# Optimization experiments

Hardware: AMD Instinct MI355X
Metric: run time of the kernel (lower is better)

Reference implementation:

```python
import jax, jax.numpy as jnp
import numpy as np

L = 8192            # sequence length
V = 100000          # vocab size
E = 256             # embedding dim
H = 512             # lstm hidden dim (bidirectional total)
HD = H // 2         # per-direction hidden
TAGS = 32
T = TAGS + 2        # tagset + START/STOP
START = T - 2       # START_TAG = -2
STOP = T - 1        # STOP_TAG = -1
NEG = -10000.0


def setup_inputs() -> dict:
    key = jax.random.key(0)
    ks = jax.random.split(key, 11)
    s = 0.05
    return {
        "input_words": jax.random.randint(ks[0], (L,), 0, V),
        "embed": jax.random.normal(ks[1], (V, E), dtype=jnp.float32) * s,
        "Wih_f": jax.random.normal(ks[2], (4 * HD, E), dtype=jnp.float32) * s,
        "Whh_f": jax.random.normal(ks[3], (4 * HD, HD), dtype=jnp.float32) * s,
        "b_f": jax.random.normal(ks[4], (4 * HD,), dtype=jnp.float32) * s,
        "Wih_b": jax.random.normal(ks[5], (4 * HD, E), dtype=jnp.float32) * s,
        "Whh_b": jax.random.normal(ks[6], (4 * HD, HD), dtype=jnp.float32) * s,
        "b_b": jax.random.normal(ks[7], (4 * HD,), dtype=jnp.float32) * s,
        "W_out": jax.random.normal(ks[8], (T, H), dtype=jnp.float32) * s,
        "b_out": jax.random.normal(ks[9], (T,), dtype=jnp.float32) * s,
        "transitions": jax.random.normal(ks[10], (T, T), dtype=jnp.float32),
    }


def _lstm_dir(x, Wih, Whh, b, reverse):
    # single-layer LSTM, one direction; torch gate order i, f, g, o
    def step(carry, xt):
        h, c = carry
        g = xt @ Wih.T + h @ Whh.T + b
        i, f, gg, o = jnp.split(g, 4)
        i = jax.nn.sigmoid(i)
        f = jax.nn.sigmoid(f)
        gg = jnp.tanh(gg)
        o = jax.nn.sigmoid(o)
        c = f * c + i * gg
        h = o * jnp.tanh(c)
        return (h, c), h

    init = (jnp.zeros((HD,), x.dtype), jnp.zeros((HD,), x.dtype))
    _, hs = jax.lax.scan(step, init, x, reverse=reverse)
    return hs  # (L, HD)


def _crf_marginals(feats, transitions):
    lse = jax.nn.logsumexp
    # forward algorithm: alpha_t[j] = lse_i(alpha_{t-1}[i] + trans[j,i]) + feat_t[j]
    def fstep(alpha, feat):
        new = lse(alpha[None, :] + transitions, axis=1) + feat
        return new, new

    alpha0 = jnp.full((T,), NEG, feats.dtype).at[START].set(0.0)
    alphaL, log_alpha = jax.lax.scan(fstep, alpha0, feats)  # (L, T)

    # backward algorithm, replicating repo's init: beta_L[j] = lse_i(trans[i, j])
    beta_last = lse(transitions, axis=0)

    # beta_t[j] = lse_i(beta_{t+1}[i] + feat_{t+1}[i] + trans[i, j])
    def bstep(beta, feat_next):
        new = lse((beta + feat_next)[:, None] + transitions, axis=0)
        return new, new

    _, betas = jax.lax.scan(bstep, beta_last, feats[1:], reverse=True)
    log_beta = jnp.concatenate([betas, beta_last[None]], axis=0)  # (L, T)
    return log_alpha + log_beta


def reference(input_words, embed, Wih_f, Whh_f, b_f, Wih_b, Whh_b, b_b,
              W_out, b_out, transitions):
    x = embed[input_words]                           # (L, E)
    hf = _lstm_dir(x, Wih_f, Whh_f, b_f, reverse=False)
    hb = _lstm_dir(x, Wih_b, Whh_b, b_b, reverse=True)
    lstm_out = jnp.concatenate([hf, hb], axis=-1)    # (L, H)
    feats = lstm_out @ W_out.T + b_out               # (L, T)
    score = _crf_marginals(feats, transitions)       # (L, T)
    tags = jnp.argmax(score, axis=1)                 # (L,)
    return score, tags
```

## Files before the change

kernel.cpp:

```cpp
#include <hip/hip_runtime.h>
#include <cstdint>
#include <cstddef>

#define LSEQ 8192
#define NT   34
#define NP   36
#define SCH  64
#define CCH  128
#define F_L2E 1.4426950408889634f
#define F_LN2 0.6931471805599453f

#if __has_builtin(__builtin_amdgcn_sdot4)
#define DOT4(a,b,c) __builtin_amdgcn_sdot4((a),(b),(c),false)
#else
__device__ __forceinline__ int dot4_fb(int a,int b,int c){
  c += (int)(signed char)(a & 0xff)        * (int)(signed char)(b & 0xff);
  c += (int)(signed char)((a>>8) & 0xff)   * (int)(signed char)((b>>8) & 0xff);
  c += (int)(signed char)((a>>16) & 0xff)  * (int)(signed char)((b>>16) & 0xff);
  c += (a>>24) * (b>>24);
  return c;
}
#define DOT4(a,b,c) dot4_fb((a),(b),(c))
#endif

__device__ __forceinline__ float ex2(float x){
#if __has_builtin(__builtin_amdgcn_exp2f)
  return __builtin_amdgcn_exp2f(x);
#else
  return exp2f(x);
#endif
}
__device__ __forceinline__ float lg2(float x){
#if __has_builtin(__builtin_amdgcn_logf)
  return __builtin_amdgcn_logf(x);
#else
  return __log2f(x);
#endif
}

__device__ __forceinline__ float sigf(float x){
  return __fdividef(1.f, 1.f + ex2(-F_L2E * x));
}
__device__ __forceinline__ float tanhf_fast(float x){
  return 1.f - __fdividef(2.f, ex2(2.f * F_L2E * x) + 1.f);
}

__device__ __forceinline__ void barrier_lds(){
  asm volatile("s_waitcnt lgkmcnt(0)\n\ts_barrier" ::: "memory");
}

__global__ void k_quant(const float* __restrict__ Whh_f,
                        const float* __restrict__ Whh_b,
                        int* __restrict__ Wq, float* __restrict__ fac){
  int bid = blockIdx.x;
  int dir = bid >> 10;
  int r   = bid & 1023;
  int i   = threadIdx.x;
  const float* W = (dir ? Whh_b : Whh_f) + r * 256 + i * 4;
  float w0 = W[0], w1 = W[1], w2 = W[2], w3 = W[3];
  float m = fmaxf(fmaxf(fabsf(w0), fabsf(w1)), fmaxf(fabsf(w2), fabsf(w3)));
  for (int s = 32; s; s >>= 1) m = fmaxf(m, __shfl_xor(m, s));
  float scale = (m > 0.f) ? m / 127.f : 1.f;
  float inv = __fdividef(1.f, scale);
  int q0 = (int)rintf(w0 * inv), q1 = (int)rintf(w1 * inv);
  int q2 = (int)rintf(w2 * inv), q3 = (int)rintf(w3 * inv);
  q0 = max(-127, min(127, q0)); q1 = max(-127, min(127, q1));
  q2 = max(-127, min(127, q2)); q3 = max(-127, min(127, q3));
  int p = (q0 & 255) | ((q1 & 255) << 8) | ((q2 & 255) << 16) | ((q3 & 255) << 24);
  Wq[(dir << 16) + (r << 6) + i] = p;
  if (i == 0) fac[(dir << 10) + r] = scale * (1.f / 127.f);
}

__global__ void k_gproj(const int* __restrict__ words,
                        const float* __restrict__ embed,
                        const float* __restrict__ Wih_f, const float* __restrict__ b_f,
                        const float* __restrict__ Wih_b, const float* __restrict__ b_b,
                        float* __restrict__ G_f, float* __restrict__ G_b){
  int dir = blockIdx.y;
  const float* Wih = dir ? Wih_b : Wih_f;
  const float* bb  = dir ? b_b  : b_f;
  float* G = dir ? G_b : G_f;
  int t0 = blockIdx.x * 16;
  __shared__ __align__(16) float X[16 * 256];
  for (int idx = threadIdx.x; idx < 16 * 256; idx += 256) {
    int tt = idx >> 8, e = idx & 255;
    X[idx] = embed[(size_t)words[t0 + tt] * 256 + e];
  }
  __syncthreads();
  const float4* X4 = (const float4*)X;
  for (int rb = 0; rb < 4; rb++) {
    int r = rb * 256 + threadIdx.x;
    float bv = bb[r];
    float acc[16];
#pragma unroll
    for (int tt = 0; tt < 16; tt++) acc[tt] = bv;
    const float4* W4 = (const float4*)(Wih + (size_t)r * 256);
    for (int eb = 0; eb < 64; eb++) {
      float4 w = W4[eb];
#pragma unroll
      for (int tt = 0; tt < 16; tt++) {
        float4 x = X4[tt * 64 + eb];
        acc[tt] += w.x * x.x + w.y * x.y + w.z * x.z + w.w * x.w;
      }
    }
    for (int tt = 0; tt < 16; tt++)
      G[(size_t)(t0 + tt) * 1024 + r] = acc[tt];
  }
}

__global__ __launch_bounds__(512, 2) void k_lstm(const int* __restrict__ Wq,
                                                 const float* __restrict__ fac,
                                                 const float* __restrict__ G_f,
                                                 const float* __restrict__ G_b,
                                                 float* __restrict__ hf,
                                                 float* __restrict__ hb){
  int dir = blockIdx.x;
  const int4* Wq4 = (const int4*)(Wq + (dir << 16));
  const float* facp = fac + (dir << 10);
  const float* G = dir ? G_b : G_f;
  float* hout = dir ? hb : hf;
  int tid = threadIdx.x;

  __shared__ __align__(16) int h8[64];
  __shared__ float graw[1024];

  int4 wA[16], wB[16];
#pragma unroll
  for (int i = 0; i < 16; i++) {
    wA[i] = Wq4[tid * 16 + i];
    wB[i] = Wq4[(tid + 512) * 16 + i];
  }
  float fA = facp[tid], fB = facp[tid + 512];
  if (tid < 64) h8[tid] = 0;
  float c = 0.f;

  float ga0 = 0, ga1 = 0, ga2 = 0, ga3 = 0;
  float gb0 = 0, gb1 = 0, gb2 = 0, gb3 = 0;
  if (tid < 256) {
    int tm0 = dir ? 8191 : 0;
    int tm1 = dir ? 8190 : 1;
    const float* p0 = G + (size_t)tm0 * 1024 + tid;
    ga0 = p0[0]; ga1 = p0[256]; ga2 = p0[512]; ga3 = p0[768];
    const float* p1 = G + (size_t)tm1 * 1024 + tid;
    gb0 = p1[0]; gb1 = p1[256]; gb2 = p1[512]; gb3 = p1[768];
  }
  __syncthreads();

  auto step = [&](int t, float& g0, float& g1, float& g2, float& g3) {
    float pa0 = 0, pa1 = 0, pa2 = 0, pa3 = 0;
    if (tid < 256) {
      int tn = t + 2; if (tn > 8191) tn = 8191;
      int time2 = dir ? (8191 - tn) : tn;
      const float* p = G + (size_t)time2 * 1024 + tid;
      pa0 = p[0]; pa1 = p[256]; pa2 = p[512]; pa3 = p[768];
    }
    int accA = 0, accB = 0;
    const int4* h84 = (const int4*)h8;
#pragma unroll
    for (int i = 0; i < 16; ++i) {
      int4 hv = h84[i];
      accA = DOT4(wA[i].x, hv.x, accA); accA = DOT4(wA[i].y, hv.y, accA);
      accA = DOT4(wA[i].z, hv.z, accA); accA = DOT4(wA[i].w, hv.w, accA);
      accB = DOT4(wB[i].x, hv.x, accB); accB = DOT4(wB[i].y, hv.y, accB);
      accB = DOT4(wB[i].z, hv.z, accB); accB = DOT4(wB[i].w, hv.w, accB);
    }
    graw[tid]       = (float)accA * fA;
    graw[tid + 512] = (float)accB * fB;
    barrier_lds();
    if (tid < 256) {
      int time = dir ? (8191 - t) : t;
      float ri = graw[tid]       + g0;
      float rf = graw[256 + tid] + g1;
      float rg = graw[512 + tid] + g2;
      float ro = graw[768 + tid] + g3;
      float is = sigf(ri), fs = sigf(rf);
      float gt = tanhf_fast(rg), os = sigf(ro);
      c = fs * c + is * gt;
      float h = os * tanhf_fast(c);
      hout[(size_t)time * 256 + tid] = h;
      ((signed char*)h8)[tid] = (signed char)(int)rintf(h * 127.f);
    }
    g0 = pa0; g1 = pa1; g2 = pa2; g3 = pa3;
    barrier_lds();
  };

  for (int t = 0; t < 8192; t += 2) {
    step(t,     ga0, ga1, ga2, ga3);
    step(t + 1, gb0, gb1, gb2, gb3);
  }
}

__global__ void k_feats(const float* __restrict__ hf, const float* __restrict__ hb,
                        const float* __restrict__ W_out, const float* __restrict__ b_out,
                        float* __restrict__ feats){
  int t0 = blockIdx.x * 16;
  for (int oi = threadIdx.x; oi < 16 * NT; oi += 256) {
    int tt = oi / NT;
    int tag = oi - tt * NT;
    int t = t0 + tt;
    const float4* w4 = (const float4*)(W_out + (size_t)tag * 512);
    const float4* a4 = (const float4*)(hf + (size_t)t * 256);
    const float4* c4 = (const float4*)(hb + (size_t)t * 256);
    float acc = b_out[tag];
    for (int k = 0; k < 64; k++) {
      float4 w = w4[k]; float4 h = a4[k];
      acc += w.x * h.x + w.y * h.y + w.z * h.z + w.w * h.w;
    }
    for (int k = 0; k < 64; k++) {
      float4 w = w4[64 + k]; float4 h = c4[k];
      acc += w.x * h.x + w.y * h.y + w.z * h.z + w.w * h.w;
    }
    feats[(size_t)t * NT + tag] = acc;
  }
}

__global__ __launch_bounds__(320) void k_crf_p1(const float* __restrict__ feats,
                                                const float* __restrict__ trans,
                                                float* __restrict__ Pg,
                                                float* __restrict__ rmaxG){
  int dir = blockIdx.x >> 7;
  int c   = blockIdx.x & (CCH - 1);
  int tid = threadIdx.x;
  int t0  = c * SCH;

  __shared__ __align__(16) float TRM[NT * NP];
  __shared__ float Fe[(SCH + 1) * NT];
  __shared__ __align__(16) float Pbuf[2][NT * NP];
  __shared__ float CM[NP];
  __shared__ float RMs[NT];

  for (int idx = tid; idx < NT * NT; idx += 320) {
    int j = idx / NT, k = idx - j * NT;
    float v = (dir == 0) ? trans[j * NT + k] : trans[k * NT + j];
    TRM[j * NP + k] = v * F_L2E;
  }
  for (int idx = tid; idx < (SCH + 1) * NT; idx += 320) {
    int s = idx / NT, j = idx - s * NT;
    int t = t0 + s; if (t > LSEQ - 1) t = LSEQ - 1;
    Fe[idx] = feats[(size_t)t * NT + j] * F_L2E;
  }
  for (int idx = tid; idx < NT * NP; idx += 320) {
    int k = idx / NP, i = idx - k * NP;
    Pbuf[0][idx] = (i < NT && i == k) ? 0.f : -1e30f;
  }
  if (tid < NP) CM[tid] = (tid < NT) ? 0.f : -1e30f;
  __syncthreads();
  if (tid < NT) {
    float m = -3e38f;
    for (int k = 0; k < NT; k++) m = fmaxf(m, TRM[tid * NP + k]);
    RMs[tid] = m;
  }
  __syncthreads();
  for (int idx = tid; idx < NT * NT; idx += 320) {
    int j = idx / NT, k = idx - j * NT;
    TRM[j * NP + k] -= RMs[j];
  }
  __syncthreads();

  int cur = 0;
  int j = tid / 9, g = tid - (tid / 9) * 9;
  bool act = (tid < 306);
  int i0 = 4 * g;

  for (int s = 0; s < SCH; s++) {
    int t = (dir == 0) ? (t0 + s) : (t0 + SCH - 1 - s);
    if (dir == 1 && t == LSEQ - 1) continue;
    const float* Pc = Pbuf[cur];
    float* Pn = Pbuf[cur ^ 1];
    if (act) {
      float cm0 = CM[i0], cm1 = CM[i0 + 1], cm2 = CM[i0 + 2], cm3 = CM[i0 + 3];
      float s0 = 0, s1 = 0, s2 = 0, s3 = 0;
      const float* trp = TRM + j * NP;
      const float* fep = Fe + (t + 1 - t0) * NT;
#pragma unroll
      for (int k = 0; k < NT; k++) {
        float trv = trp[k];
        if (dir == 1) trv += fep[k];
        float4 p = *(const float4*)&Pc[k * NP + i0];
        s0 += ex2(trv + p.x - cm0);
        s1 += ex2(trv + p.y - cm1);
        s2 += ex2(trv + p.z - cm2);
        s3 += ex2(trv + p.w - cm3);
      }
      float base = RMs[j] + ((dir == 0) ? Fe[(t - t0) * NT + j] : 0.f);
      float4 o;
      o.x = base + cm0 + lg2(s0);
      o.y = base + cm1 + lg2(s1);
      o.z = (i0 + 2 < NT) ? (base + cm2 + lg2(s2)) : -1e30f;
      o.w = (i0 + 3 < NT) ? (base + cm3 + lg2(s3)) : -1e30f;
      *(float4*)&Pn[j * NP + i0] = o;
    }
    __syncthreads();
    if (tid < NP) {
      float m = -3e38f;
      const float* col = Pn + tid;
      for (int k = 0; k < NT; k++) m = fmaxf(m, col[k * NP]);
      CM[tid] = m;
    }
    cur ^= 1;
    __syncthreads();
  }

  const float* Pf = Pbuf[cur];
  size_t base = (size_t)((dir << 7) + c) * (NT * NP);
  for (int idx = tid; idx < NT * NP; idx += 320)
    Pg[base + idx] = Pf[idx];
  if (tid < NT) {
    float m = -3e38f;
    for (int i = 0; i < NT; i++) m = fmaxf(m, Pf[tid * NP + i]);
    rmaxG[((dir << 7) + c) * NT + tid] = m;
  }
}

__global__ void k_crf_p2(const float* __restrict__ trans,
                         const float* __restrict__ Pg,
                         const float* __restrict__ rmaxG,
                         float* __restrict__ vIn){
  int dir = blockIdx.x;
  int lane = threadIdx.x;
  bool a = (lane < NT);
  int j = a ? lane : 0;
  __shared__ float V[NP];

  float v;
  if (dir == 0) {
    v = (lane == 32) ? 0.f : -10000.f * F_L2E;
  } else {
    float m = -3e38f;
    for (int i = 0; i < NT; i++) m = fmaxf(m, trans[i * NT + j]);
    float s = 0.f;
    for (int i = 0; i < NT; i++) s += ex2((trans[i * NT + j] - m) * F_L2E);
    v = m * F_L2E + lg2(s);
  }
  if (lane < NP) V[lane] = -1e30f;
  barrier_lds();
  if (a) V[j] = v;
  barrier_lds();
  float vm = a ? v : -3e38f;
  for (int off = 32; off; off >>= 1) vm = fmaxf(vm, __shfl_xor(vm, off));

  if (a) {
    int c0 = (dir == 0) ? 0 : (CCH - 1);
    vIn[((size_t)(dir << 7) + c0) * NP + j] = v;
  }

  for (int it = 0; it < CCH - 1; it++) {
    int c = (dir == 0) ? it : (CCH - 1 - it);
    const float* row = Pg + ((size_t)(dir << 7) + c) * (NT * NP) + j * NP;
    float rm = rmaxG[((dir << 7) + c) * NT + j];
    float m = rm + vm;
    float s = 0.f;
#pragma unroll
    for (int k = 0; k < NP; k += 4) {
      float4 p = *(const float4*)&row[k];
      s += ex2(p.x + V[k]     - m);
      s += ex2(p.y + V[k + 1] - m);
      s += ex2(p.z + V[k + 2] - m);
      s += ex2(p.w + V[k + 3] - m);
    }
    float nv = m + lg2(s);
    if (a) V[j] = nv;
    barrier_lds();
    float x = a ? nv : -3e38f;
    for (int off = 32; off; off >>= 1) x = fmaxf(x, __shfl_xor(x, off));
    vm = x;
    int cn = (dir == 0) ? (c + 1) : (c - 1);
    if (a) vIn[((size_t)(dir << 7) + cn) * NP + j] = nv;
  }
}

__global__ void k_crf_p3(const float* __restrict__ feats,
                         const float* __restrict__ trans,
                         const float* __restrict__ vIn,
                         float* __restrict__ wsA,
                         float* __restrict__ wsB){
  int dir = blockIdx.x >> 7;
  int c   = blockIdx.x & (CCH - 1);
  int lane = threadIdx.x;
  int t0 = c * SCH;
  bool a = (lane < NT);
  int j = a ? lane : 0;
  __shared__ float A[NP];
  __shared__ float U[NP];

  float trr[NT];
  float rm = -3e38f;
#pragma unroll
  for (int k = 0; k < NT; k++) {
    float vv = (dir == 0) ? trans[j * NT + k] : trans[k * NT + j];
    trr[k] = vv * F_L2E;
    rm = fmaxf(rm, trr[k]);
  }
  if (lane < NP) { A[lane] = -1e30f; U[lane] = -1e30f; }
  float v0 = vIn[((size_t)(dir << 7) + c) * NP + j];
  barrier_lds();
  if (a) A[j] = v0;
  barrier_lds();
  float am = a ? v0 : -3e38f;
  for (int off = 32; off; off >>= 1) am = fmaxf(am, __shfl_xor(am, off));

  if (dir == 0) {
    float fe = feats[(size_t)t0 * NT + j] * F_L2E;
    for (int s = 0; s < SCH; s++) {
      int t = t0 + s;
      int tn = (t + 1 < LSEQ) ? t + 1 : LSEQ - 1;
      float fe_n = feats[(size_t)tn * NT + j] * F_L2E;
      float m = rm + am;
      float ss = 0.f;
#pragma unroll
      for (int k = 0; k < NT; k++) ss += ex2(trr[k] + A[k] - m);
      float out = m + lg2(ss) + fe;
      if (a) wsA[(size_t)t * NT + j] = out * F_LN2;
      if (a) A[j] = out;
      barrier_lds();
      float x = a ? out : -3e38f;
      for (int off = 32; off; off >>= 1) x = fmaxf(x, __shfl_xor(x, off));
      am = x;
      fe = fe_n;
    }
  } else {
    float b = v0;
    int tfirst = t0 + SCH; if (tfirst > LSEQ - 1) tfirst = LSEQ - 1;
    float fe = feats[(size_t)tfirst * NT + j] * F_L2E;
    for (int s = 0; s < SCH; s++) {
      int t = t0 + SCH - 1 - s;
      float fe_n = feats[(size_t)t * NT + j] * F_L2E;
      float out;
      if (t == LSEQ - 1) {
        out = b;
      } else {
        if (a) U[j] = b + fe;
        barrier_lds();
        float um = a ? U[j] : -3e38f;
        for (int off = 32; off; off >>= 1) um = fmaxf(um, __shfl_xor(um, off));
        float m = rm + um;
        float ss = 0.f;
#pragma unroll
        for (int k = 0; k < NT; k++) ss += ex2(trr[k] + U[k] - m);
        out = m + lg2(ss);
        barrier_lds();
      }
      if (a) wsB[(size_t)t * NT + j] = out * F_LN2;
      b = out;
      fe = fe_n;
    }
  }
}

__global__ void k_finish(const float* __restrict__ wsA, const float* __restrict__ wsB,
                         float* __restrict__ out){
  int t = blockIdx.x * 256 + threadIdx.x;
  float m = -3e38f; int bi = 0;
  for (int i = 0; i < NT; i++) {
    float sc = wsA[(size_t)t * NT + i] + wsB[(size_t)t * NT + i];
    out[(size_t)t * NT + i] = sc;
    if (sc > m) { m = sc; bi = i; }
  }
  out[(size_t)LSEQ * NT + t] = (float)bi;
}

extern "C" void kernel_launch(void* const* d_in, const int* in_sizes, int n_in,
                              void* d_out, int out_size, void* d_ws, size_t ws_size,
                              hipStream_t stream) {
  const int*   words  = (const int*)  d_in[0];
  const float* embed  = (const float*)d_in[1];
  const float* Wih_f  = (const float*)d_in[2];
  const float* Whh_f  = (const float*)d_in[3];
  const float* b_f    = (const float*)d_in[4];
  const float* Wih_b  = (const float*)d_in[5];
  const float* Whh_b  = (const float*)d_in[6];
  const float* b_b    = (const float*)d_in[7];
  const float* W_out  = (const float*)d_in[8];
  const float* b_out  = (const float*)d_in[9];
  const float* trans  = (const float*)d_in[10];
  float* out = (float*)d_out;

  float* wsf = (float*)d_ws;
  size_t off = 0;
  float* G_f   = wsf + off; off += (size_t)LSEQ * 1024;
  float* G_b   = wsf + off; off += (size_t)LSEQ * 1024;
  float* hf    = wsf + off; off += (size_t)LSEQ * 256;
  float* hb    = wsf + off; off += (size_t)LSEQ * 256;
  float* feats = wsf + off; off += (size_t)LSEQ * NT + 16;
  float* wsA   = wsf + off; off += (size_t)LSEQ * NT + 16;
  float* wsB   = wsf + off; off += (size_t)LSEQ * NT + 16;
  float* fac   = wsf + off; off += 2048;
  int*   Wq    = (int*)(wsf + off); off += 2 * 1024 * 64;
  float* Pg    = G_f;
  float* rmaxG = G_f + 256 * (NT * NP);
  float* vIn   = rmaxG + 256 * NT + 32;

  k_quant<<<2048, 64, 0, stream>>>(Whh_f, Whh_b, Wq, fac);
  k_gproj<<<dim3(512, 2), 256, 0, stream>>>(words, embed, Wih_f, b_f, Wih_b, b_b, G_f, G_b);
  k_lstm<<<2, 512, 0, stream>>>(Wq, fac, G_f, G_b, hf, hb);
  k_feats<<<512, 256, 0, stream>>>(hf, hb, W_out, b_out, feats);
  k_crf_p1<<<256, 320, 0, stream>>>(feats, trans, Pg, rmaxG);
  k_crf_p2<<<2, 64, 0, stream>>>(trans, Pg, rmaxG, vIn);
  k_crf_p3<<<256, 64, 0, stream>>>(feats, trans, vIn, wsA, wsB);
  k_finish<<<32, 256, 0, stream>>>(wsA, wsB, out);
}
```

Before: 8.583 ms.

## Use int8 MFMA for LSTM recurrence with gate-interleaved layout and double-buffered h

Rewrites the sequential LSTM kernel so the recurrent int8 matvec runs on 16x16x64 i8 MFMA instructions, with weight fragments held in registers. The gate projection output and the quantization scales are re-laid out so each hidden unit's four gates sit contiguously, which lets one thread load a float4 of gate inputs. The quantized hidden state is double-buffered in LDS, dropping one barrier and the graw LDS round-trip per step. This trades the dot4 path for MFMA, which computes a 16-wide matrix-vector product and wastes most columns, and it adds select logic to extract each unit's result. It also drops the builtin exp2/log intrinsics in favour of the generic exp2f/__log2f.

After: 9.312 ms. 8.5% more time.

```diff
diff --git a/kernel.cpp b/kernel.cpp
--- a/kernel.cpp
+++ b/kernel.cpp
@@ -10,33 +10,10 @@
 #define F_L2E 1.4426950408889634f
 #define F_LN2 0.6931471805599453f
 
-#if __has_builtin(__builtin_amdgcn_sdot4)
-#define DOT4(a,b,c) __builtin_amdgcn_sdot4((a),(b),(c),false)
-#else
-__device__ __forceinline__ int dot4_fb(int a,int b,int c){
-  c += (int)(signed char)(a & 0xff)        * (int)(signed char)(b & 0xff);
-  c += (int)(signed char)((a>>8) & 0xff)   * (int)(signed char)((b>>8) & 0xff);
-  c += (int)(signed char)((a>>16) & 0xff)  * (int)(signed char)((b>>16) & 0xff);
-  c += (a>>24) * (b>>24);
-  return c;
-}
-#define DOT4(a,b,c) dot4_fb((a),(b),(c))
-#endif
-
-__device__ __forceinline__ float ex2(float x){
-#if __has_builtin(__builtin_amdgcn_exp2f)
-  return __builtin_amdgcn_exp2f(x);
-#else
-  return exp2f(x);
-#endif
-}
-__device__ __forceinline__ float lg2(float x){
-#if __has_builtin(__builtin_amdgcn_logf)
-  return __builtin_amdgcn_logf(x);
-#else
-  return __log2f(x);
-#endif
-}
+typedef int v4i __attribute__((ext_vector_type(4)));
+
+__device__ __forceinline__ float ex2(float x){ return exp2f(x); }
+__device__ __forceinline__ float lg2(float x){ return __log2f(x); }
 
 __device__ __forceinline__ float sigf(float x){
   return __fdividef(1.f, 1.f + ex2(-F_L2E * x));
@@ -51,7 +28,7 @@
 
 __global__ void k_quant(const float* __restrict__ Whh_f,
                         const float* __restrict__ Whh_b,
-                        int* __restrict__ Wq, float* __restrict__ fac){
+                        int* __restrict__ Wq, float* __restrict__ facP){
   int bid = blockIdx.x;
   int dir = bid >> 10;
   int r   = bid & 1023;
@@ -68,7 +45,10 @@
   q2 = max(-127, min(127, q2)); q3 = max(-127, min(127, q3));
   int p = (q0 & 255) | ((q1 & 255) << 8) | ((q2 & 255) << 16) | ((q3 & 255) << 24);
   Wq[(dir << 16) + (r << 6) + i] = p;
-  if (i == 0) fac[(dir << 10) + r] = scale * (1.f / 127.f);
+  if (i == 0) {
+    int g = r >> 8, u = r & 255;
+    facP[(dir << 10) + u * 4 + g] = scale * (1.f / 127.f);
+  }
 }
 
 __global__ void k_gproj(const int* __restrict__ words,
@@ -81,6 +61,7 @@
   const float* bb  = dir ? b_b  : b_f;
   float* G = dir ? G_b : G_f;
   int t0 = blockIdx.x * 16;
+  int uu = threadIdx.x;
   __shared__ __align__(16) float X[16 * 256];
   for (int idx = threadIdx.x; idx < 16 * 256; idx += 256) {
     int tt = idx >> 8, e = idx & 255;
@@ -88,105 +69,114 @@
   }
   __syncthreads();
   const float4* X4 = (const float4*)X;
-  for (int rb = 0; rb < 4; rb++) {
-    int r = rb * 256 + threadIdx.x;
-    float bv = bb[r];
-    float acc[16];
-#pragma unroll
-    for (int tt = 0; tt < 16; tt++) acc[tt] = bv;
-    const float4* W4 = (const float4*)(Wih + (size_t)r * 256);
+  const float4* Wr0 = (const float4*)(Wih + (size_t)(uu)       * 256);
+  const float4* Wr1 = (const float4*)(Wih + (size_t)(uu + 256) * 256);
+  const float4* Wr2 = (const float4*)(Wih + (size_t)(uu + 512) * 256);
+  const float4* Wr3 = (const float4*)(Wih + (size_t)(uu + 768) * 256);
+  float b0 = bb[uu], b1 = bb[uu + 256], b2 = bb[uu + 512], b3 = bb[uu + 768];
+  for (int pass = 0; pass < 2; pass++) {
+    float4 acc[8];
+#pragma unroll
+    for (int tt = 0; tt < 8; tt++) acc[tt] = make_float4(b0, b1, b2, b3);
     for (int eb = 0; eb < 64; eb++) {
-      float4 w = W4[eb];
-#pragma unroll
-      for (int tt = 0; tt < 16; tt++) {
-        float4 x = X4[tt * 64 + eb];
-        acc[tt] += w.x * x.x + w.y * x.y + w.z * x.z + w.w * x.w;
+      float4 w0 = Wr0[eb], w1 = Wr1[eb], w2 = Wr2[eb], w3 = Wr3[eb];
+#pragma unroll
+      for (int tt = 0; tt < 8; tt++) {
+        float4 x = X4[(pass * 8 + tt) * 64 + eb];
+        acc[tt].x += w0.x * x.x + w0.y * x.y + w0.z * x.z + w0.w * x.w;
+        acc[tt].y += w1.x * x.x + w1.y * x.y + w1.z * x.z + w1.w * x.w;
+        acc[tt].z += w2.x * x.x + w2.y * x.y + w2.z * x.z + w2.w * x.w;
+        acc[tt].w += w3.x * x.x + w3.y * x.y + w3.z * x.z + w3.w * x.w;
       }
     }
-    for (int tt = 0; tt < 16; tt++)
-      G[(size_t)(t0 + tt) * 1024 + r] = acc[tt];
-  }
-}
-
-__global__ __launch_bounds__(512, 2) void k_lstm(const int* __restrict__ Wq,
-                                                 const float* __restrict__ fac,
-                                                 const float* __restrict__ G_f,
-                                                 const float* __restrict__ G_b,
-                                                 float* __restrict__ hf,
-                                                 float* __restrict__ hb){
+#pragma unroll
+    for (int tt = 0; tt < 8; tt++)
+      *(float4*)(G + (size_t)(t0 + pass * 8 + tt) * 1024 + uu * 4) = acc[tt];
+  }
+}
+
+__global__ __launch_bounds__(512, 2) void k_lstm3(const int* __restrict__ Wq,
+                                                  const float* __restrict__ facP,
+                                                  const float* __restrict__ G_f,
+                                                  const float* __restrict__ G_b,
+                                                  float* __restrict__ hf,
+                                                  float* __restrict__ hb){
   int dir = blockIdx.x;
-  const int4* Wq4 = (const int4*)(Wq + (dir << 16));
-  const float* facp = fac + (dir << 10);
+  const int* Wqd = Wq + (dir << 16);
   const float* G = dir ? G_b : G_f;
   float* hout = dir ? hb : hf;
   int tid = threadIdx.x;
-
-  __shared__ __align__(16) int h8[64];
-  __shared__ float graw[1024];
-
-  int4 wA[16], wB[16];
-#pragma unroll
-  for (int i = 0; i < 16; i++) {
-    wA[i] = Wq4[tid * 16 + i];
-    wB[i] = Wq4[(tid + 512) * 16 + i];
-  }
-  float fA = facp[tid], fB = facp[tid + 512];
-  if (tid < 64) h8[tid] = 0;
+  int w = tid >> 6, L = tid & 63;
+  int m = L & 15, q = L >> 4, T = L & 7, col = L & 15;
+  int u = w * 32 + T * 4 + q;
+
+  __shared__ int h8[2 * 64];
+
+  v4i afr[8][4];
+#pragma unroll
+  for (int t8 = 0; t8 < 8; t8++) {
+    int r_orig = (m & 3) * 256 + (w * 32 + t8 * 4 + (m >> 2));
+    const int* base = Wqd + r_orig * 64;
+#pragma unroll
+    for (int kt = 0; kt < 4; kt++) {
+      int4 tmp = *(const int4*)(base + kt * 16 + q * 4);
+      afr[t8][kt] = (v4i){tmp.x, tmp.y, tmp.z, tmp.w};
+    }
+  }
+  float4 fv = *(const float4*)(facP + (dir << 10) + u * 4);
+  int time0 = dir ? 8191 : 0;
+  float4 gcur = *(const float4*)(G + (size_t)time0 * 1024 + u * 4);
+
+  if (tid < 128) h8[tid] = 0;
   float c = 0.f;
-
-  float ga0 = 0, ga1 = 0, ga2 = 0, ga3 = 0;
-  float gb0 = 0, gb1 = 0, gb2 = 0, gb3 = 0;
-  if (tid < 256) {
-    int tm0 = dir ? 8191 : 0;
-    int tm1 = dir ? 8190 : 1;
-    const float* p0 = G + (size_t)tm0 * 1024 + tid;
-    ga0 = p0[0]; ga1 = p0[256]; ga2 = p0[512]; ga3 = p0[768];
-    const float* p1 = G + (size_t)tm1 * 1024 + tid;
-    gb0 = p1[0]; gb1 = p1[256]; gb2 = p1[512]; gb3 = p1[768];
-  }
   __syncthreads();
 
-  auto step = [&](int t, float& g0, float& g1, float& g2, float& g3) {
-    float pa0 = 0, pa1 = 0, pa2 = 0, pa3 = 0;
-    if (tid < 256) {
-      int tn = t + 2; if (tn > 8191) tn = 8191;
-      int time2 = dir ? (8191 - tn) : tn;
-      const float* p = G + (size_t)time2 * 1024 + tid;
-      pa0 = p[0]; pa1 = p[256]; pa2 = p[512]; pa3 = p[768];
-    }
-    int accA = 0, accB = 0;
-    const int4* h84 = (const int4*)h8;
-#pragma unroll
-    for (int i = 0; i < 16; ++i) {
-      int4 hv = h84[i];
-      accA = DOT4(wA[i].x, hv.x, accA); accA = DOT4(wA[i].y, hv.y, accA);
-      accA = DOT4(wA[i].z, hv.z, accA); accA = DOT4(wA[i].w, hv.w, accA);
-      accB = DOT4(wB[i].x, hv.x, accB); accB = DOT4(wB[i].y, hv.y, accB);
-      accB = DOT4(wB[i].z, hv.z, accB); accB = DOT4(wB[i].w, hv.w, accB);
-    }
-    graw[tid]       = (float)accA * fA;
-    graw[tid + 512] = (float)accB * fB;
+  for (int t = 0; t < 8192; t++) {
+    int tn = (t + 1 < 8192) ? t + 1 : 8191;
+    int time_n = dir ? (8191 - tn) : tn;
+    float4 gnext = *(const float4*)(G + (size_t)time_n * 1024 + u * 4);
+
+    int p = t & 1;
+    const char* rb = (const char*)h8 + p * 256;
+    v4i bfr[4];
+#pragma unroll
+    for (int kt = 0; kt < 4; kt++) {
+      int4 tmp = *(const int4*)(rb + kt * 64 + q * 16);
+      bfr[kt] = (v4i){tmp.x, tmp.y, tmp.z, tmp.w};
+    }
+    v4i acc[8];
+#pragma unroll
+    for (int t8 = 0; t8 < 8; t8++) {
+      v4i a = (v4i){0, 0, 0, 0};
+#pragma unroll
+      for (int kt = 0; kt < 4; kt++)
+        a = __builtin_amdgcn_mfma_i32_16x16x64_i8(afr[t8][kt], bfr[kt], a, 0, 0, 0);
+      acc[t8] = a;
+    }
+    v4i x0 = (T & 1) ? acc[1] : acc[0];
+    v4i x1 = (T & 1) ? acc[3] : acc[2];
+    v4i x2 = (T & 1) ? acc[5] : acc[4];
+    v4i x3 = (T & 1) ? acc[7] : acc[6];
+    v4i y0 = (T & 2) ? x1 : x0;
+    v4i y1 = (T & 2) ? x3 : x2;
+    v4i d  = (T & 4) ? y1 : y0;
+
+    float ri = (float)d[0] * fv.x + gcur.x;
+    float rf = (float)d[1] * fv.y + gcur.y;
+    float rg = (float)d[2] * fv.z + gcur.z;
+    float ro = (float)d[3] * fv.w + gcur.w;
+    float is = sigf(ri), fs = sigf(rf);
+    float gt = tanhf_fast(rg), os = sigf(ro);
+    c = fs * c + is * gt;
+    float h = os * tanhf_fast(c);
+
+    int time = dir ? (8191 - t) : t;
+    if (col < 8) {
+      hout[(size_t)time * 256 + u] = h;
+      ((signed char*)h8)[(p ^ 1) * 256 + u] = (signed char)(int)rintf(h * 127.f);
+    }
+    gcur = gnext;
     barrier_lds();
-    if (tid < 256) {
-      int time = dir ? (8191 - t) : t;
-      float ri = graw[tid]       + g0;
-      float rf = graw[256 + tid] + g1;
-      float rg = graw[512 + tid] + g2;
-      float ro = graw[768 + tid] + g3;
-      float is = sigf(ri), fs = sigf(rf);
-      float gt = tanhf_fast(rg), os = sigf(ro);
-      c = fs * c + is * gt;
-      float h = os * tanhf_fast(c);
-      hout[(size_t)time * 256 + tid] = h;
-      ((signed char*)h8)[tid] = (signed char)(int)rintf(h * 127.f);
-    }
-    g0 = pa0; g1 = pa1; g2 = pa2; g3 = pa3;
-    barrier_lds();
-  };
-
-  for (int t = 0; t < 8192; t += 2) {
-    step(t,     ga0, ga1, ga2, ga3);
-    step(t + 1, gb0, gb1, gb2, gb3);
   }
 }
 
@@ -293,8 +283,8 @@
     __syncthreads();
     if (tid < NP) {
       float m = -3e38f;
-      const float* col = Pn + tid;
-      for (int k = 0; k < NT; k++) m = fmaxf(m, col[k * NP]);
+      const float* colp = Pn + tid;
+      for (int k = 0; k < NT; k++) m = fmaxf(m, colp[k * NP]);
       CM[tid] = m;
     }
     cur ^= 1;
@@ -484,15 +474,15 @@
   float* feats = wsf + off; off += (size_t)LSEQ * NT + 16;
   float* wsA   = wsf + off; off += (size_t)LSEQ * NT + 16;
   float* wsB   = wsf + off; off += (size_t)LSEQ * NT + 16;
-  float* fac   = wsf + off; off += 2048;
+  float* facP  = wsf + off; off += 2048;
   int*   Wq    = (int*)(wsf + off); off += 2 * 1024 * 64;
   float* Pg    = G_f;
   float* rmaxG = G_f + 256 * (NT * NP);
   float* vIn   = rmaxG + 256 * NT + 32;
 
-  k_quant<<<2048, 64, 0, stream>>>(Whh_f, Whh_b, Wq, fac);
+  k_quant<<<2048, 64, 0, stream>>>(Whh_f, Whh_b, Wq, facP);
   k_gproj<<<dim3(512, 2), 256, 0, stream>>>(words, embed, Wih_f, b_f, Wih_b, b_b, G_f, G_b);
-  k_lstm<<<2, 512, 0, stream>>>(Wq, fac, G_f, G_b, hf, hb);
+  k_lstm3<<<2, 512, 0, stream>>>(Wq, facP, G_f, G_b, hf, hb);
   k_feats<<<512, 256, 0, stream>>>(hf, hb, W_out, b_out, feats);
   k_crf_p1<<<256, 320, 0, stream>>>(feats, trans, Pg, rmaxG);
   k_crf_p2<<<2, 64, 0, stream>>>(trans, Pg, rmaxG, vIn);
```
